# Performance work log

Measured on AMD Instinct MI355X. Metric: run time of the kernel, lower is better.

The kernel has to match this reference:

```python
import jax, jax.numpy as jnp
import numpy as np

B, S, DM1, DM2, DK, DV = 8, 2048, 768, 768, 64, 64
EPS = 1e-5


def setup_inputs() -> dict:
    key = jax.random.key(0)
    ks = jax.random.split(key, 8)
    s1 = 1.0 / np.sqrt(DM1)
    s2 = 1.0 / np.sqrt(DM2)
    return {
        "x_1": jax.random.normal(ks[0], (B, S, DM1), jnp.float32),
        "x_2": jax.random.normal(ks[1], (B, S, DM2), jnp.float32),
        "Wq": jax.random.uniform(ks[2], (DM1, DK), jnp.float32, -s1, s1),
        "bq": jnp.zeros((DK,), jnp.float32),
        "Wk": jax.random.uniform(ks[3], (DM2, DK), jnp.float32, -s2, s2),
        "bk": jnp.zeros((DK,), jnp.float32),
        "Wv": jax.random.uniform(ks[4], (DM2, DV), jnp.float32, -s2, s2),
        "bv": jnp.zeros((DV,), jnp.float32),
        "gamma": jnp.ones((DV,), jnp.float32),
        "beta": jnp.zeros((DV,), jnp.float32),
    }


def reference(x_1, x_2, Wq, bq, Wk, bk, Wv, bv, gamma, beta):
    q = jnp.einsum("bsd,dk->bsk", x_1, Wq) + bq            # [B,S,DK]
    k = jnp.einsum("bsd,dk->bsk", x_2, Wk) + bk            # [B,S,DK]
    v = jnp.einsum("bsd,dv->bsv", x_2, Wv) + bv            # [B,S,DV]
    scores = jnp.einsum("bqk,bsk->bqs", q, k) / jnp.sqrt(jnp.float32(DK))
    w = jax.nn.softmax(scores, axis=-1)                    # [B,S,S]
    # reverse-weight transform (reverse=True)
    dim = w.shape[1]
    w = (1.0 - w) / (dim - 1)
    attn = jnp.einsum("bqs,bsv->bqv", w, v)                # [B,S,DV]
    mu = jnp.mean(attn, axis=-1, keepdims=True)
    var = jnp.var(attn, axis=-1, keepdims=True)
    out = (attn - mu) * jax.lax.rsqrt(var + EPS) * gamma + beta
    return out
```

## Files before the change

### kernel.cpp

```cpp
#include <hip/hip_runtime.h>
#include <hip/hip_bf16.h>

#define BATCH 8
#define SEQ   2048
#define DM    768
#define DD    64
#define BS (BATCH * SEQ)
#define SCALEQ 0.1803369380478f

typedef __bf16 bf16x8 __attribute__((ext_vector_type(8)));
typedef float  f32x4  __attribute__((ext_vector_type(4)));
typedef short  short8 __attribute__((ext_vector_type(8)));
typedef short  short4v __attribute__((ext_vector_type(4)));

#define MFMA16(a, b, c) __builtin_amdgcn_mfma_f32_16x16x32_bf16((a), (b), (c), 0, 0, 0)

__device__ __forceinline__ short f2bf(float x) {
    unsigned u = __builtin_bit_cast(unsigned, x);
    u = (u + 0x7fffu + ((u >> 16) & 1u)) >> 16;
    return (short)u;
}
__device__ __forceinline__ float bf2f(short s) {
    unsigned u = ((unsigned)(unsigned short)s) << 16;
    return __builtin_bit_cast(float, u);
}
__device__ __forceinline__ bf16x8 cvt8(float4 a, float4 b) {
    bf16x8 r;
    r[0] = (__bf16)a.x; r[1] = (__bf16)a.y; r[2] = (__bf16)a.z; r[3] = (__bf16)a.w;
    r[4] = (__bf16)b.x; r[5] = (__bf16)b.y; r[6] = (__bf16)b.z; r[7] = (__bf16)b.w;
    return r;
}
__device__ __forceinline__ void gld16(const void* g, void* l) {
    __builtin_amdgcn_global_load_lds(
        (const __attribute__((address_space(1))) void*)g,
        (__attribute__((address_space(3))) void*)l, 16, 0, 0);
}

__global__ void prep_w_kernel(const float* __restrict__ Wq, const float* __restrict__ Wk,
                              const float* __restrict__ Wv, short* __restrict__ Wt,
                              float* __restrict__ C) {
    int idx = blockIdx.x * 256 + threadIdx.x;
    if (idx < BATCH * DD) C[idx] = 0.f;
    if (idx >= 3 * DM * DD) return;
    int m = idx / (DM * DD);
    int r = (idx % (DM * DD)) / DD;
    int c = idx % DD;
    const float* W = (m == 0) ? Wq : (m == 1) ? Wk : Wv;
    float scale = (m == 0) ? SCALEQ : 1.0f;
    Wt[m * DM * DD + c * DM + r] = f2bf(W[r * DD + c] * scale);
}

__global__ __launch_bounds__(256, 2) void proj_kernel(
        const float* __restrict__ x1, const float* __restrict__ x2,
        const short* __restrict__ Wt,
        const float* __restrict__ bq, const float* __restrict__ bk,
        const float* __restrict__ bv,
        short* __restrict__ Qs, short* __restrict__ Kb, short* __restrict__ Vtb,
        float* __restrict__ C) {
    __shared__ __align__(16) float als[2][64 * 32];
    __shared__ __align__(16) short wls[2][2][2048];
    const int tid = threadIdx.x, wave = tid >> 6, lane = tid & 63;
    const int quad = lane >> 4, l15 = lane & 15;
    const int kv = blockIdx.x & 1;
    const int r0 = (blockIdx.x >> 1) * 64;
    const float* x = kv ? x2 : x1;
    const int m0 = kv ? 1 : 0;

    const int sg = wave * 2;
    const int arow0 = sg * 8 + (lane >> 3);
    const int aswz = ((lane & 7) ^ ((lane >> 3) & 7)) * 4;
    const float* asrc0 = x + (size_t)(r0 + arow0) * DM + aswz;
    const float* asrc1 = asrc0 + (size_t)8 * DM;
    const short* wsrc0 = Wt + (size_t)(m0 * DD + lane) * DM + wave * 8;
    const short* wsrc1 = Wt + (size_t)(2  * DD + lane) * DM + wave * 8;

    f32x4 acc0[4] = {}, acc1[4] = {};

    gld16(asrc0, &als[0][sg * 256]);
    gld16(asrc1, &als[0][(sg + 1) * 256]);
    gld16(wsrc0, &wls[0][0][wave * 512]);
    if (kv) gld16(wsrc1, &wls[0][1][wave * 512]);
    __syncthreads();

    const int arow = wave * 16 + l15;
    const int s0 = (((quad * 2) ^ (l15 & 7))) * 4;
    const int s1 = (((quad * 2 + 1) ^ (l15 & 7))) * 4;

    for (int p = 0; p < 24; p++) {
        const int cur = p & 1;
        if (p + 1 < 24) {
            gld16(asrc0 + (p + 1) * 32, &als[cur ^ 1][sg * 256]);
            gld16(asrc1 + (p + 1) * 32, &als[cur ^ 1][(sg + 1) * 256]);
            gld16(wsrc0 + (p + 1) * 32, &wls[cur ^ 1][0][wave * 512]);
            if (kv) gld16(wsrc1 + (p + 1) * 32, &wls[cur ^ 1][1][wave * 512]);
        }
        float4 a0 = *(const float4*)&als[cur][arow * 32 + s0];
        float4 a1 = *(const float4*)&als[cur][arow * 32 + s1];
        bf16x8 af = cvt8(a0, a1);
#pragma unroll
        for (int tn = 0; tn < 4; tn++) {
            bf16x8 w0 = *(const bf16x8*)&wls[cur][0][(quad * 64 + tn * 16 + l15) * 8];
            acc0[tn] = MFMA16(af, w0, acc0[tn]);
            if (kv) {
                bf16x8 w1 = *(const bf16x8*)&wls[cur][1][(quad * 64 + tn * 16 + l15) * 8];
                acc1[tn] = MFMA16(af, w1, acc1[tn]);
            }
        }
        __syncthreads();
    }

    if (!kv) {
#pragma unroll
        for (int tn = 0; tn < 4; tn++) {
            int v = tn * 16 + l15;
            float bb = bq[v] * SCALEQ;
#pragma unroll
            for (int r = 0; r < 4; r++)
                Qs[(size_t)(r0 + wave * 16 + quad * 4 + r) * DD + v] = f2bf(acc0[tn][r] + bb);
        }
    } else {
#pragma unroll
        for (int tn = 0; tn < 4; tn++) {
            int v = tn * 16 + l15;
            float bb = bk[v];
#pragma unroll
            for (int r = 0; r < 4; r++)
                Kb[(size_t)(r0 + wave * 16 + quad * 4 + r) * DD + v] = f2bf(acc0[tn][r] + bb);
        }
        const int b = r0 / SEQ;
        const int sbase = (r0 % SEQ) + wave * 16 + quad * 4;
#pragma unroll
        for (int tn = 0; tn < 4; tn++) {
            int v = tn * 16 + l15;
            float bb = bv[v];
            short4v pk;
            float cs = 0.f;
#pragma unroll
            for (int r = 0; r < 4; r++) {
                pk[r] = f2bf(acc1[tn][r] + bb);
                cs += bf2f(pk[r]);
            }
            *(short4v*)(Vtb + ((size_t)b * DD + v) * SEQ + sbase) = pk;
            cs += __shfl_xor(cs, 16);
            cs += __shfl_xor(cs, 32);
            if (quad == 0) atomicAdd(&C[b * DD + v], cs);
        }
    }
}

#define PBS 72
__global__ __launch_bounds__(256, 2) void flash_kernel(
        const short* __restrict__ Q, const short* __restrict__ K,
        const short* __restrict__ Vt,
        short* __restrict__ Yp, float* __restrict__ Dp) {
    __shared__ __align__(16) short pbuf[4][64 * PBS];
    __shared__ float dl[4][64];
    const int tid  = threadIdx.x;
    const int wave = tid >> 6, lane = tid & 63, quad = lane >> 4, l15 = lane & 15;
    const int blk = blockIdx.x;
    const int b = blk & 7, qt = (blk >> 3) & 31, half = blk >> 8;
    const int q0 = qt * 64;

    bf16x8 qf[4][2];
#pragma unroll
    for (int qn = 0; qn < 4; qn++)
#pragma unroll
        for (int kc = 0; kc < 2; kc++)
            qf[qn][kc] = *(const bf16x8*)(Q + ((size_t)(b * SEQ + q0 + qn * 16 + l15)) * DD
                                          + kc * 32 + quad * 8);

    const short* Kbp = K  + (size_t)b * SEQ * DD;
    const short* Vbp = Vt + (size_t)b * DD * SEQ;
    f32x4 y[4][4] = {};
    float den[4] = {0.f, 0.f, 0.f, 0.f};
    short* pw = &pbuf[wave][0];

    const int s_begin = half * 1024 + wave * 256;
    for (int s0 = s_begin; s0 < s_begin + 256; s0 += 64) {
#pragma unroll
        for (int tn = 0; tn < 4; tn++) {
            const short* kf = Kbp + (size_t)(s0 + tn * 16 + l15) * DD + quad * 8;
            bf16x8 ka0 = *(const bf16x8*)kf;
            bf16x8 ka1 = *(const bf16x8*)(kf + 32);
#pragma unroll
            for (int qn = 0; qn < 4; qn++) {
                f32x4 z = {0.f, 0.f, 0.f, 0.f};
                z = MFMA16(ka0, qf[qn][0], z);
                z = MFMA16(ka1, qf[qn][1], z);
                short4v pk;
#pragma unroll
                for (int r = 0; r < 4; r++) {
                    float p = __builtin_amdgcn_exp2f(z[r]);
                    den[qn] += p;
                    pk[r] = f2bf(p);
                }
                *(short4v*)&pw[(qn * 16 + l15) * PBS + tn * 16 + quad * 4] = pk;
            }
        }
#pragma unroll
        for (int kc = 0; kc < 2; kc++) {
            bf16x8 pB[4];
#pragma unroll
            for (int qn = 0; qn < 4; qn++)
                pB[qn] = *(const bf16x8*)&pw[(qn * 16 + l15) * PBS + kc * 32 + quad * 8];
#pragma unroll
            for (int vn = 0; vn < 4; vn++) {
                bf16x8 va = *(const bf16x8*)(Vbp + (size_t)(vn * 16 + l15) * SEQ
                                             + s0 + kc * 32 + quad * 8);
#pragma unroll
                for (int qn = 0; qn < 4; qn++)
                    y[qn][vn] = MFMA16(va, pB[qn], y[qn][vn]);
            }
        }
    }
#pragma unroll
    for (int qn = 0; qn < 4; qn++) {
        den[qn] += __shfl_xor(den[qn], 16);
        den[qn] += __shfl_xor(den[qn], 32);
    }
#pragma unroll
    for (int qn = 0; qn < 4; qn++) {
#pragma unroll
        for (int vn = 0; vn < 4; vn++) {
            short4v pk;
#pragma unroll
            for (int r = 0; r < 4; r++) pk[r] = f2bf(y[qn][vn][r]);
            *(short4v*)&pw[(qn * 16 + l15) * PBS + vn * 16 + quad * 4] = pk;
        }
        if (quad == 0) dl[wave][qn * 16 + l15] = den[qn];
    }
    __syncthreads();
    {
        const int q = wave * 16 + l15;
        float D = dl[0][q] + dl[1][q] + dl[2][q] + dl[3][q];
        float ys[16];
#pragma unroll
        for (int j = 0; j < 16; j++) ys[j] = 0.f;
#pragma unroll
        for (int u = 0; u < 4; u++) {
#pragma unroll
            for (int h = 0; h < 2; h++) {
                bf16x8 t = *(const bf16x8*)&pbuf[u][q * PBS + quad * 16 + h * 8];
#pragma unroll
                for (int j = 0; j < 8; j++) ys[h * 8 + j] += (float)t[j];
            }
        }
        const size_t row = (size_t)b * SEQ + q0 + q;
        short8 o0, o1;
#pragma unroll
        for (int j = 0; j < 8; j++) { o0[j] = f2bf(ys[j]); o1[j] = f2bf(ys[8 + j]); }
        short* yout = Yp + ((size_t)half * BS + row) * DD + quad * 16;
        *(short8*)yout = o0;
        *(short8*)(yout + 8) = o1;
        if (quad == 0) Dp[half * BS + row] = D;
    }
}

__global__ __launch_bounds__(256) void reduce_ln_kernel(
        const short* __restrict__ Yp, const float* __restrict__ Dp,
        const float* __restrict__ C, const float* __restrict__ gamma,
        const float* __restrict__ beta, float* __restrict__ out) {
    const int row = blockIdx.x * 4 + (threadIdx.x >> 6);
    const int v = threadIdx.x & 63;
    const int b = row >> 11;
    float Y = bf2f(Yp[(size_t)row * DD + v]) + bf2f(Yp[((size_t)BS + row) * DD + v]);
    float D = Dp[row] + Dp[BS + row];
    float attn = (C[b * DD + v] - Y / D) * (1.0f / (float)(SEQ - 1));
    float msum = attn, ssum = attn * attn;
#pragma unroll
    for (int m = 1; m < 64; m <<= 1) {
        msum += __shfl_xor(msum, m);
        ssum += __shfl_xor(ssum, m);
    }
    float mu = msum * (1.0f / 64.0f);
    float var = ssum * (1.0f / 64.0f) - mu * mu;
    float rs = rsqrtf(var + 1e-5f);
    out[(size_t)row * DD + v] = (attn - mu) * rs * gamma[v] + beta[v];
}

extern "C" void kernel_launch(void* const* d_in, const int* in_sizes, int n_in,
                              void* d_out, int out_size, void* d_ws, size_t ws_size,
                              hipStream_t stream) {
    const float* x1    = (const float*)d_in[0];
    const float* x2    = (const float*)d_in[1];
    const float* Wq    = (const float*)d_in[2];
    const float* bq    = (const float*)d_in[3];
    const float* Wk    = (const float*)d_in[4];
    const float* bk    = (const float*)d_in[5];
    const float* Wv    = (const float*)d_in[6];
    const float* bv    = (const float*)d_in[7];
    const float* gamma = (const float*)d_in[8];
    const float* beta  = (const float*)d_in[9];
    float* out = (float*)d_out;

    char* ws = (char*)d_ws;
    short* Qs  = (short*)(ws);
    short* Kbf = (short*)(ws + (2ull << 20));
    short* Vtb = (short*)(ws + (4ull << 20));
    short* Wt  = (short*)(ws + (6ull << 20));
    float* Cc  = (float*)(ws + (6ull << 20) + 3 * DM * DD * 2);
    short* Yp  = (short*)(ws + (7ull << 20));
    float* Dp  = (float*)(ws + (11ull << 20));

    prep_w_kernel<<<576, 256, 0, stream>>>(Wq, Wk, Wv, Wt, Cc);
    proj_kernel<<<512, 256, 0, stream>>>(x1, x2, Wt, bq, bk, bv, Qs, Kbf, Vtb, Cc);
    flash_kernel<<<512, 256, 0, stream>>>(Qs, Kbf, Vtb, Yp, Dp);
    reduce_ln_kernel<<<BS / 4, 256, 0, stream>>>(Yp, Dp, Cc, gamma, beta, out);
}
```

Baseline: 181.6 us.

## Deepen projection kernel global-to-LDS pipeline to four stages with vmcnt waits

The projection kernel's double-buffered LDS staging becomes a 4-deep ring, keeping three tiles in flight. Explicit s_waitcnt vmcnt counts plus raw s_barrier replace the per-iteration __syncthreads, and the loop is split by the kv branch so the wait counts are uniform. The goal is to hide global load latency in this memory-bound projection. In exchange LDS use doubles (about 64KB per block), which may cut occupancy below the two-blocks-per-CU target. Correctness relies on the hand-picked wait counts matching how many loads each stage issues.

```diff
diff --git a/kernel.cpp b/kernel.cpp
--- a/kernel.cpp
+++ b/kernel.cpp
@@ -57,8 +57,8 @@
         const float* __restrict__ bv,
         short* __restrict__ Qs, short* __restrict__ Kb, short* __restrict__ Vtb,
         float* __restrict__ C) {
-    __shared__ __align__(16) float als[2][64 * 32];
-    __shared__ __align__(16) short wls[2][2][2048];
+    __shared__ __align__(16) float als[4][64 * 32];
+    __shared__ __align__(16) short wls[4][2][2048];
     const int tid = threadIdx.x, wave = tid >> 6, lane = tid & 63;
     const int quad = lane >> 4, l15 = lane & 15;
     const int kv = blockIdx.x & 1;
@@ -76,40 +76,43 @@
 
     f32x4 acc0[4] = {}, acc1[4] = {};
 
-    gld16(asrc0, &als[0][sg * 256]);
-    gld16(asrc1, &als[0][(sg + 1) * 256]);
-    gld16(wsrc0, &wls[0][0][wave * 512]);
-    if (kv) gld16(wsrc1, &wls[0][1][wave * 512]);
-    __syncthreads();
-
     const int arow = wave * 16 + l15;
-    const int s0 = (((quad * 2) ^ (l15 & 7))) * 4;
-    const int s1 = (((quad * 2 + 1) ^ (l15 & 7))) * 4;
-
-    for (int p = 0; p < 24; p++) {
-        const int cur = p & 1;
-        if (p + 1 < 24) {
-            gld16(asrc0 + (p + 1) * 32, &als[cur ^ 1][sg * 256]);
-            gld16(asrc1 + (p + 1) * 32, &als[cur ^ 1][(sg + 1) * 256]);
-            gld16(wsrc0 + (p + 1) * 32, &wls[cur ^ 1][0][wave * 512]);
-            if (kv) gld16(wsrc1 + (p + 1) * 32, &wls[cur ^ 1][1][wave * 512]);
-        }
-        float4 a0 = *(const float4*)&als[cur][arow * 32 + s0];
-        float4 a1 = *(const float4*)&als[cur][arow * 32 + s1];
-        bf16x8 af = cvt8(a0, a1);
-#pragma unroll
-        for (int tn = 0; tn < 4; tn++) {
-            bf16x8 w0 = *(const bf16x8*)&wls[cur][0][(quad * 64 + tn * 16 + l15) * 8];
-            acc0[tn] = MFMA16(af, w0, acc0[tn]);
-            if (kv) {
-                bf16x8 w1 = *(const bf16x8*)&wls[cur][1][(quad * 64 + tn * 16 + l15) * 8];
-                acc1[tn] = MFMA16(af, w1, acc1[tn]);
-            }
-        }
-        __syncthreads();
-    }
+    const int s0 = ((quad * 2) ^ (l15 & 7)) * 4;
+    const int s1 = ((quad * 2 + 1) ^ (l15 & 7)) * 4;
+
+#define PROJ_WAIT(N)                                         \
+    asm volatile("s_waitcnt vmcnt(" #N ")" ::: "memory");    \
+    __builtin_amdgcn_sched_barrier(0);                       \
+    __builtin_amdgcn_s_barrier();
 
     if (!kv) {
+        auto STAGE = [&](int t) {
+            float* ab = &als[t & 3][0];
+            gld16(asrc0 + t * 32, ab + sg * 256);
+            gld16(asrc1 + t * 32, ab + (sg + 1) * 256);
+            gld16(wsrc0 + t * 32, &wls[t & 3][0][wave * 512]);
+        };
+        auto COMP = [&](int p) {
+            const float* ab = &als[p & 3][0];
+            float4 a0 = *(const float4*)(ab + arow * 32 + s0);
+            float4 a1 = *(const float4*)(ab + arow * 32 + s1);
+            bf16x8 af = cvt8(a0, a1);
+            const short* wb = &wls[p & 3][0][0];
+#pragma unroll
+            for (int tn = 0; tn < 4; tn++)
+                acc0[tn] = MFMA16(af, *(const bf16x8*)(wb + (quad * 64 + tn * 16 + l15) * 8),
+                                  acc0[tn]);
+        };
+        STAGE(0); STAGE(1); STAGE(2);
+        for (int p = 0; p < 21; ++p) {
+            STAGE(p + 3);
+            PROJ_WAIT(9)
+            COMP(p);
+            __builtin_amdgcn_s_barrier();
+        }
+        PROJ_WAIT(6)  COMP(21); __builtin_amdgcn_s_barrier();
+        PROJ_WAIT(3)  COMP(22); __builtin_amdgcn_s_barrier();
+        PROJ_WAIT(0)  COMP(23);
 #pragma unroll
         for (int tn = 0; tn < 4; tn++) {
             int v = tn * 16 + l15;
@@ -119,6 +122,37 @@
                 Qs[(size_t)(r0 + wave * 16 + quad * 4 + r) * DD + v] = f2bf(acc0[tn][r] + bb);
         }
     } else {
+        auto STAGE = [&](int t) {
+            float* ab = &als[t & 3][0];
+            gld16(asrc0 + t * 32, ab + sg * 256);
+            gld16(asrc1 + t * 32, ab + (sg + 1) * 256);
+            gld16(wsrc0 + t * 32, &wls[t & 3][0][wave * 512]);
+            gld16(wsrc1 + t * 32, &wls[t & 3][1][wave * 512]);
+        };
+        auto COMP = [&](int p) {
+            const float* ab = &als[p & 3][0];
+            float4 a0 = *(const float4*)(ab + arow * 32 + s0);
+            float4 a1 = *(const float4*)(ab + arow * 32 + s1);
+            bf16x8 af = cvt8(a0, a1);
+            const short* wb0 = &wls[p & 3][0][0];
+            const short* wb1 = &wls[p & 3][1][0];
+#pragma unroll
+            for (int tn = 0; tn < 4; tn++) {
+                const int fo = (quad * 64 + tn * 16 + l15) * 8;
+                acc0[tn] = MFMA16(af, *(const bf16x8*)(wb0 + fo), acc0[tn]);
+                acc1[tn] = MFMA16(af, *(const bf16x8*)(wb1 + fo), acc1[tn]);
+            }
+        };
+        STAGE(0); STAGE(1); STAGE(2);
+        for (int p = 0; p < 21; ++p) {
+            STAGE(p + 3);
+            PROJ_WAIT(12)
+            COMP(p);
+            __builtin_amdgcn_s_barrier();
+        }
+        PROJ_WAIT(8)  COMP(21); __builtin_amdgcn_s_barrier();
+        PROJ_WAIT(4)  COMP(22); __builtin_amdgcn_s_barrier();
+        PROJ_WAIT(0)  COMP(23);
 #pragma unroll
         for (int tn = 0; tn < 4; tn++) {
             int v = tn * 16 + l15;
@@ -146,6 +180,7 @@
             if (quad == 0) atomicAdd(&C[b * DD + v], cs);
         }
     }
+#undef PROJ_WAIT
 }
 
 #define PBS 72
```

After: 178.8 us. About the same (-1.5%).
